# Kernel optimization log

Measured on AMD Instinct MI355X. Metric: run time of the kernel, lower is better.

## Reference

```python
import jax, jax.numpy as jnp
import numpy as np

H_DIM = 512
FF_DIM = 2048
N_HEAD = 4
N_BLOCK = 3
N_TOKEN = 128
B, S = 8, 1024
LN_EPS = 1e-5


def _layernorm(x, g, b):
    mu = jnp.mean(x, axis=-1, keepdims=True)
    var = jnp.mean(jnp.square(x - mu), axis=-1, keepdims=True)
    return (x - mu) * jax.lax.rsqrt(var + LN_EPS) * g + b


def setup_inputs() -> dict:
    key = jax.random.key(0)
    ks = jax.random.split(key, 20)
    sc = 0.02
    inp = {
        'input_ids': jax.random.randint(ks[0], (B, S), 0, N_TOKEN, dtype=jnp.int32),
        'attention_mask': jnp.ones((B, S), dtype=jnp.int32),
        'emb': jax.random.uniform(ks[1], (N_TOKEN, H_DIM), dtype=jnp.float32),
        'wq': jax.random.normal(ks[2], (N_BLOCK, N_HEAD, H_DIM, H_DIM), dtype=jnp.float32) * sc,
        'wk': jax.random.normal(ks[3], (N_BLOCK, N_HEAD, H_DIM, H_DIM), dtype=jnp.float32) * sc,
        'wv': jax.random.normal(ks[4], (N_BLOCK, N_HEAD, H_DIM, H_DIM), dtype=jnp.float32) * sc,
        'wo_w': jax.random.normal(ks[5], (N_BLOCK, N_HEAD * H_DIM, H_DIM), dtype=jnp.float32) * sc,
        'wo_b': jnp.zeros((N_BLOCK, H_DIM), dtype=jnp.float32),
        'ln1_g': jnp.ones((N_BLOCK, H_DIM), dtype=jnp.float32),
        'ln1_b': jnp.zeros((N_BLOCK, H_DIM), dtype=jnp.float32),
        'ff1_w': jax.random.normal(ks[6], (N_BLOCK, FF_DIM, H_DIM), dtype=jnp.float32) * sc,
        'ff1_b': jnp.zeros((N_BLOCK, FF_DIM), dtype=jnp.float32),
        'ff2_w': jax.random.normal(ks[7], (N_BLOCK, H_DIM, FF_DIM), dtype=jnp.float32) * sc,
        'ff2_b': jnp.zeros((N_BLOCK, H_DIM), dtype=jnp.float32),
        'ln2_g': jnp.ones((N_BLOCK, H_DIM), dtype=jnp.float32),
        'ln2_b': jnp.zeros((N_BLOCK, H_DIM), dtype=jnp.float32),
        'lm_w': jax.random.normal(ks[8], (H_DIM, N_TOKEN), dtype=jnp.float32) * sc,
    }
    return inp


def reference(emb, wq, wk, wv, wo_w, wo_b, ln1_g, ln1_b, ff1_w, ff1_b,
              ff2_w, ff2_b, ln2_g, ln2_b, lm_w, input_ids, attention_mask):
    mask_f = attention_mask.astype(jnp.float32)          # [B,S]
    valid = attention_mask != 0                          # [B,S]

    # Embedding lookup
    x = emb[input_ids]                                   # [B,S,H]

    # Positional encoding: positions assigned sequentially to valid tokens;
    # both even and odd feature slots get the SAME sin value (per source).
    pos = jnp.cumsum(mask_f, axis=-1) - 1.0              # [B,S]
    div = jnp.exp(jnp.arange(0, H_DIM, 2, dtype=jnp.float32) * (-jnp.log(10000.0) / H_DIM))  # [H/2]
    s = jnp.sin(pos[..., None] * div)                    # [B,S,H/2]
    pos_enc = jnp.repeat(s, 2, axis=-1) * mask_f[..., None]
    x = x + pos_enc

    # Allowed attention: causal (key <= query) AND query valid AND key valid
    rows = jnp.arange(S)
    causal = rows[None, :, None] >= rows[None, None, :]  # [1,S,S] (query>=key)
    allowed = causal & valid[:, :, None] & valid[:, None, :]  # [B,S,S]
    neg_inf = jnp.float32(-jnp.inf)
    scale = jnp.sqrt(jnp.float32(H_DIM))

    for l in range(N_BLOCK):
        # Per-head full-width attention (each head uses full H_DIM)
        q = jnp.einsum('bsh,nhd->bnsd', x, wq[l])
        k = jnp.einsum('bsh,nhd->bnsd', x, wk[l])
        v = jnp.einsum('bsh,nhd->bnsd', x, wv[l])
        scores = jnp.einsum('bnsd,bntd->bnst', q, k) / scale      # [B,N,S,S]
        scores = jnp.where(allowed[:, None], scores, neg_inf)
        att = jax.nn.softmax(scores, axis=-1)
        att = jnp.where(jnp.isnan(att), 0.0, att)                  # NaN rows -> 0
        o = jnp.einsum('bnst,bntd->bnsd', att, v)                  # [B,N,S,H]
        o = jnp.transpose(o, (0, 2, 1, 3)).reshape(B, S, N_HEAD * H_DIM)
        mh = o @ wo_w[l] + wo_b[l]
        x = _layernorm(x + mh, ln1_g[l], ln1_b[l])
        # Conv1d with kernel 1 == pointwise linear
        ff = jax.nn.relu(jnp.einsum('bsh,fh->bsf', x, ff1_w[l]) + ff1_b[l])
        ff = jnp.einsum('bsf,hf->bsh', ff, ff2_w[l]) + ff2_b[l]
        x = _layernorm(x + ff, ln2_g[l], ln2_b[l])

    return x @ lm_w                                       # [B,S,N_TOKEN]
```

## Files before the change

### kernel.cpp

```cpp
#include <hip/hip_runtime.h>
#include <hip/hip_bf16.h>

#define S_LEN 1024
#define BATCH 8
#define HD 512
#define FFD 2048
#define NHEAD 4
#define NBLK 3
#define NTOK 128

typedef __bf16 bf16_t;
typedef __bf16 bf16x4_t __attribute__((ext_vector_type(4)));
typedef __bf16 bf16x8_t __attribute__((ext_vector_type(8)));
typedef float f32x4_t __attribute__((ext_vector_type(4)));

typedef __attribute__((address_space(3))) uint32_t lds_u32;
typedef __attribute__((address_space(1))) uint32_t glb_u32;

template<int NI>
__device__ __forceinline__ void ldsread(const bf16_t* __restrict__ buf, int row0,
                                        int fr, int fg, int sw, bf16x8_t (&dst)[NI][2]) {
  #pragma unroll
  for (int i = 0; i < NI; ++i)
    #pragma unroll
    for (int ks = 0; ks < 2; ++ks)
      dst[i][ks] = *(const bf16x8_t*)&buf[(row0 + i*16 + fr)*64 + (((ks*4 + fg) ^ sw) << 3)];
}

template<int IB, int JB>
__device__ __forceinline__ void mquad(f32x4_t (&acc)[8][4],
                                      const bf16x8_t (&af)[4][2], const bf16x8_t (&bf)[2][2]) {
  #pragma unroll
  for (int ks = 0; ks < 2; ++ks)
    #pragma unroll
    for (int i = 0; i < 4; ++i)
      #pragma unroll
      for (int j = 0; j < 2; ++j)
        acc[IB+i][JB+j] = __builtin_amdgcn_mfma_f32_16x16x32_bf16(af[i][ks], bf[j][ks], acc[IB+i][JB+j], 0, 0, 0);
}

template<bool OUT_BF16, bool BIAS, bool RELU, bool TRI, bool CKLIM, bool NORM>
__global__ __launch_bounds__(512, 2)
void gemm256_kernel(const bf16_t* __restrict__ A,
                    const bf16_t* __restrict__ Bt,
                    const float* __restrict__ bias,
                    void* __restrict__ Cv,
                    int M, int N, int K,
                    int lda, int ldb, int ldc,
                    long long sA, long long sB, int bshift, long long sBias,
                    int zshift, long long sC_hi, long long sC_lo,
                    int msub_shift, long long msub_stride,
                    float alpha)
{
  const int zb = blockIdx.z;
  int m0, n0;
  if (TRI) {
    const int idx = blockIdx.x;
    int mi = (int)((sqrtf(8.f * idx + 1.f) - 1.f) * 0.5f);
    while ((mi + 1) * (mi + 2) / 2 <= idx) ++mi;
    while (mi * (mi + 1) / 2 > idx) --mi;
    m0 = mi * 256;
    n0 = (idx - mi * (mi + 1) / 2) * 256;
  } else {
    m0 = blockIdx.x * 256;
    n0 = blockIdx.y * 256;
  }
  int kend = K;
  if (CKLIM) { int ke = m0 + 256; kend = ke < K ? ke : K; }
  const int nt = kend >> 6;

  const bf16_t* Az = A + (long long)zb * sA;
  const bf16_t* Bz = Bt + (long long)(zb >> bshift) * sB;
  const long long coff = ((long long)(zb >> zshift)) * sC_hi
                       + ((long long)(zb & ((1 << zshift) - 1))) * sC_lo;

  __shared__ __align__(16) bf16_t As[2][256 * 64];
  __shared__ __align__(16) bf16_t Bs[2][256 * 64];

  const int tid = threadIdx.x;
  const int lane = tid & 63;
  const int w = tid >> 6;
  const int wm = (w >> 2) * 128;
  const int wn = (w & 3) * 64;
  const int fr = lane & 15;
  const int fg = lane >> 4;
  const int sw = fr & 7;

  const int srow = tid >> 3;
  const int scol8 = tid & 7;
  const int gswz = ((scol8 ^ (srow & 7)) << 3);

  f32x4_t acc[8][4];
  #pragma unroll
  for (int i = 0; i < 8; ++i)
    #pragma unroll
    for (int j = 0; j < 4; ++j)
      acc[i][j] = (f32x4_t){0.f, 0.f, 0.f, 0.f};

  const bf16_t* gA0 = Az + (long long)(m0 + srow) * lda + gswz;
  const bf16_t* gB0 = Bz + (long long)(n0 + srow) * ldb + gswz;

  auto stage_half = [&](int buf, int kt, int h) {
    if (h < 2) {
      const bf16_t* g = gA0 + (long long)(h * 128) * lda + (kt << 6);
      bf16_t* l = &As[buf][(h*128 + srow) * 64 + (scol8 << 3)];
      __builtin_amdgcn_global_load_lds((const glb_u32*)g, (lds_u32*)l, 16, 0, 0);
      __builtin_amdgcn_global_load_lds((const glb_u32*)(g + 64LL*lda), (lds_u32*)(l + 64*64), 16, 0, 0);
    } else {
      const int hh = h - 2;
      const bf16_t* g = gB0 + (long long)(hh * 128) * ldb + (kt << 6);
      bf16_t* l = &Bs[buf][(hh*128 + srow) * 64 + (scol8 << 3)];
      __builtin_amdgcn_global_load_lds((const glb_u32*)g, (lds_u32*)l, 16, 0, 0);
      __builtin_amdgcn_global_load_lds((const glb_u32*)(g + 64LL*ldb), (lds_u32*)(l + 64*64), 16, 0, 0);
    }
  };

  stage_half(0, 0, 0); stage_half(0, 0, 1); stage_half(0, 0, 2); stage_half(0, 0, 3);
  if (nt > 1) { stage_half(1, 1, 0); stage_half(1, 1, 1); }
  if (nt > 1) asm volatile("s_waitcnt vmcnt(4)" ::: "memory");
  else        asm volatile("s_waitcnt vmcnt(0)" ::: "memory");
  __builtin_amdgcn_s_barrier();
  __builtin_amdgcn_sched_barrier(0);

  for (int t = 0; t < nt; ++t) {
    const int cur = t & 1;
    const bf16_t* Ac = &As[cur][0];
    const bf16_t* Bc = &Bs[cur][0];
    bf16x8_t a0[4][2], a1[4][2], b0[2][2], b1[2][2];

    ldsread<4>(Ac, wm, fr, fg, sw, a0);
    ldsread<2>(Bc, wn, fr, fg, sw, b0);
    if (t + 1 < nt) stage_half(cur ^ 1, t + 1, 2);
    mquad<0, 0>(acc, a0, b0);
    ldsread<4>(Ac, wm + 64, fr, fg, sw, a1);
    ldsread<2>(Bc, wn + 32, fr, fg, sw, b1);
    if (t + 1 < nt) stage_half(cur ^ 1, t + 1, 3);
    mquad<4, 2>(acc, a1, b1);

    __builtin_amdgcn_s_barrier();
    __builtin_amdgcn_sched_barrier(0);

    if (t + 2 < nt) stage_half(cur, t + 2, 0);
    mquad<0, 2>(acc, a0, b1);
    if (t + 2 < nt) {
      stage_half(cur, t + 2, 1);
      asm volatile("s_waitcnt vmcnt(4)" ::: "memory");
    } else {
      asm volatile("s_waitcnt vmcnt(0)" ::: "memory");
    }
    mquad<4, 0>(acc, a1, b0);

    __builtin_amdgcn_s_barrier();
    __builtin_amdgcn_sched_barrier(0);
  }

  #pragma unroll
  for (int i = 0; i < 8; ++i) {
    #pragma unroll
    for (int e = 0; e < 4; ++e) {
      const int row = m0 + wm + i*16 + fg*4 + e;
      const long long ro = coff
        + ((long long)(row >> msub_shift)) * msub_stride
        + (long long)(row & ((1 << msub_shift) - 1)) * (long long)ldc;
      float rn = 1.f;
      if (NORM) rn = bias[(long long)zb * sBias + row];
      #pragma unroll
      for (int j = 0; j < 4; ++j) {
        const int col = n0 + wn + j*16 + fr;
        float v = acc[i][j][e] * alpha;
        if (BIAS) v += bias[(long long)zb * sBias + col];
        if (NORM) v *= rn;
        if (RELU) v = v > 0.f ? v : 0.f;
        if (OUT_BF16) ((bf16_t*)Cv)[ro + col] = (bf16_t)v;
        else          ((float*)Cv)[ro + col]  = v;
      }
    }
  }
}

template<bool OUT_BF16, bool BIAS, bool RELU, bool CSKIP, bool CKLIM>
__global__ __launch_bounds__(256, 2)
void gemm_bt_kernel(const bf16_t* __restrict__ A,
                    const bf16_t* __restrict__ Bt,
                    const float* __restrict__ bias,
                    void* __restrict__ Cv,
                    int M, int N, int K,
                    int lda, int ldb, int ldc,
                    long long sA, long long sB, int bshift, long long sBias,
                    int zshift, long long sC_hi, long long sC_lo,
                    int msub_shift, long long msub_stride,
                    float alpha)
{
  const int zb = blockIdx.z;
  const int m0 = blockIdx.x * 128;
  const int n0 = blockIdx.y * 128;
  if (CSKIP && n0 > m0 + 127) return;
  int kend = K;
  if (CKLIM) { int ke = m0 + 128; kend = ke < K ? ke : K; }

  const bf16_t* Az = A + (long long)zb * sA;
  const bf16_t* Bz = Bt + (long long)(zb >> bshift) * sB;
  const long long coff = ((long long)(zb >> zshift)) * sC_hi
                       + ((long long)(zb & ((1 << zshift) - 1))) * sC_lo;

  __shared__ __align__(16) bf16_t As[128 * 64];
  __shared__ __align__(16) bf16_t Bs[128 * 64];

  const int tid = threadIdx.x;
  const int wv = tid >> 6;
  const int lane = tid & 63;
  const int wm = (wv >> 1) * 64;
  const int wn = (wv & 1) * 64;
  const int fr = lane & 15;
  const int fg = lane >> 4;
  const int sw = fr & 7;

  f32x4_t acc[4][4];
  #pragma unroll
  for (int i = 0; i < 4; ++i)
    #pragma unroll
    for (int j = 0; j < 4; ++j)
      acc[i][j] = (f32x4_t){0.f, 0.f, 0.f, 0.f};

  const bf16_t* ga = Az + (long long)(m0 + (wv << 5) + (lane >> 3)) * lda
                   + (((lane & 7) ^ (lane >> 3)) << 3);
  const bf16_t* gb = Bz + (long long)(n0 + (wv << 5) + (lane >> 3)) * ldb
                   + (((lane & 7) ^ (lane >> 3)) << 3);

  for (int k0 = 0; k0 < kend; k0 += 64) {
    #pragma unroll
    for (int s = 0; s < 4; ++s) {
      __builtin_amdgcn_global_load_lds(
        (const glb_u32*)(ga + (long long)s * 8 * lda + k0),
        (lds_u32*)(As + (wv * 4 + s) * 512), 16, 0, 0);
      __builtin_amdgcn_global_load_lds(
        (const glb_u32*)(gb + (long long)s * 8 * ldb + k0),
        (lds_u32*)(Bs + (wv * 4 + s) * 512), 16, 0, 0);
    }
    __syncthreads();
    #pragma unroll
    for (int kc = 0; kc < 2; ++kc) {
      const int ca = ((kc * 4 + fg) ^ sw) << 3;
      bf16x8_t af[4], bfr[4];
      #pragma unroll
      for (int i = 0; i < 4; ++i)
        af[i] = *(const bf16x8_t*)&As[(wm + i*16 + fr) * 64 + ca];
      #pragma unroll
      for (int j = 0; j < 4; ++j)
        bfr[j] = *(const bf16x8_t*)&Bs[(wn + j*16 + fr) * 64 + ca];
      #pragma unroll
      for (int i = 0; i < 4; ++i)
        #pragma unroll
        for (int j = 0; j < 4; ++j)
          acc[i][j] = __builtin_amdgcn_mfma_f32_16x16x32_bf16(af[i], bfr[j], acc[i][j], 0, 0, 0);
    }
    __syncthreads();
  }

  #pragma unroll
  for (int i = 0; i < 4; ++i) {
    #pragma unroll
    for (int e = 0; e < 4; ++e) {
      const int row = m0 + wm + i*16 + fg*4 + e;
      const long long ro = coff
        + ((long long)(row >> msub_shift)) * msub_stride
        + (long long)(row & ((1 << msub_shift) - 1)) * (long long)ldc;
      #pragma unroll
      for (int j = 0; j < 4; ++j) {
        const int col = n0 + wn + j*16 + fr;
        float v = acc[i][j][e] * alpha;
        if (BIAS) v += bias[(long long)zb * sBias + col];
        if (RELU) v = v > 0.f ? v : 0.f;
        if (OUT_BF16) ((bf16_t*)Cv)[ro + col] = (bf16_t)v;
        else          ((float*)Cv)[ro + col]  = v;
      }
    }
  }
}

__global__ void softmax_kernel(bf16_t* __restrict__ scP,
                               const int* __restrict__ mask, int pair0)
{
  const int lane = threadIdx.x & 63;
  const int s = blockIdx.x * 4 + (threadIdx.x >> 6);
  const int pz = blockIdx.y;
  const int b = (pair0 + pz) >> 2;
  bf16_t* row = scP + ((long long)pz * S_LEN + s) * S_LEN;
  const int t0 = lane * 16;

  bf16x8_t r0 = *(const bf16x8_t*)&row[t0];
  bf16x8_t r1 = *(const bf16x8_t*)&row[t0 + 8];
  int4 m4[4];
  #pragma unroll
  for (int q = 0; q < 4; ++q) m4[q] = *(const int4*)&mask[b * S_LEN + t0 + q*4];
  const int* mm = (const int*)m4;

  float v[16]; bool ok[16];
  #pragma unroll
  for (int j = 0; j < 16; ++j) {
    const int t = t0 + j;
    ok[j] = (t <= s) && (mm[j] != 0);
    float raw = (j < 8) ? (float)r0[j] : (float)r1[j - 8];
    v[j] = ok[j] ? raw : -INFINITY;
  }
  float mx = v[0];
  #pragma unroll
  for (int j = 1; j < 16; ++j) mx = fmaxf(mx, v[j]);
  #pragma unroll
  for (int o = 32; o; o >>= 1) mx = fmaxf(mx, __shfl_xor(mx, o));

  float e[16]; float sum = 0.f;
  #pragma unroll
  for (int j = 0; j < 16; ++j) { e[j] = ok[j] ? __expf(v[j] - mx) : 0.f; sum += e[j]; }
  #pragma unroll
  for (int o = 32; o; o >>= 1) sum += __shfl_xor(sum, o);

  const bool qvalid = mask[b * S_LEN + s] != 0;
  const float inv = (qvalid && sum > 0.f) ? 1.f / sum : 0.f;
  bf16x8_t o0, o1;
  #pragma unroll
  for (int j = 0; j < 8; ++j) { o0[j] = (bf16_t)(e[j] * inv); o1[j] = (bf16_t)(e[j+8] * inv); }
  *(bf16x8_t*)&row[t0] = o0;
  *(bf16x8_t*)&row[t0 + 8] = o1;
}

template<typename TIN>
__global__ void transpose_kernel(const TIN* __restrict__ in, bf16_t* __restrict__ out,
                                 int R, int C, long long sIn, long long sOut)
{
  __shared__ float tile[32][33];
  const long long zi = (long long)blockIdx.z * sIn;
  const long long zo = (long long)blockIdx.z * sOut;
  const int c0 = blockIdx.x * 32, r0 = blockIdx.y * 32;
  const int tx = threadIdx.x, ty = threadIdx.y;
  #pragma unroll
  for (int i = 0; i < 4; ++i) {
    int r = r0 + ty + i*8;
    tile[ty + i*8][tx] = (float)in[zi + (long long)r * C + c0 + tx];
  }
  __syncthreads();
  #pragma unroll
  for (int i = 0; i < 4; ++i) {
    int c = c0 + ty + i*8;
    out[zo + (long long)c * R + r0 + tx] = (bf16_t)tile[tx][ty + i*8];
  }
}

__global__ void convert2_kernel(const float* __restrict__ a, const float* __restrict__ b,
                                bf16_t* __restrict__ out, long long n)
{
  long long i = (long long)blockIdx.x * blockDim.x + threadIdx.x;
  long long stride = (long long)gridDim.x * blockDim.x;
  for (; i < 2*n; i += stride)
    out[i] = (bf16_t)(i < n ? a[i] : b[i - n]);
}

__global__ void fill_kernel(float* __restrict__ out, long long n, float v)
{
  long long i = (long long)blockIdx.x * blockDim.x + threadIdx.x;
  long long stride = (long long)gridDim.x * blockDim.x;
  for (; i < n; i += stride) out[i] = v;
}

__global__ void pos_kernel(const int* __restrict__ mask, float* __restrict__ pos)
{
  __shared__ float scn[S_LEN];
  const int b = blockIdx.x, t = threadIdx.x;
  scn[t] = (float)(mask[b * S_LEN + t] != 0);
  __syncthreads();
  for (int off = 1; off < S_LEN; off <<= 1) {
    float add = (t >= off) ? scn[t - off] : 0.f;
    __syncthreads();
    scn[t] += add;
    __syncthreads();
  }
  pos[b * S_LEN + t] = scn[t] - 1.0f;
}

__global__ void embed_kernel(const int* __restrict__ ids, const int* __restrict__ mask,
                             const float* __restrict__ pos, const float* __restrict__ emb,
                             float* __restrict__ x, bf16_t* __restrict__ xb)
{
  const int idx = blockIdx.x * 256 + threadIdx.x;
  const int i = idx & 255;
  const int bs = idx >> 8;
  const int id = ids[bs];
  const float m = (float)(mask[bs] != 0);
  const float p = pos[bs];
  const float dv = __expf(-(float)(2 * i) * (9.210340371976184f / (float)HD));
  const float sv = __sinf(p * dv) * m;
  const float e0 = emb[id * HD + 2*i], e1 = emb[id * HD + 2*i + 1];
  const float x0 = e0 + sv, x1 = e1 + sv;
  x[(long long)bs * HD + 2*i]     = x0;
  x[(long long)bs * HD + 2*i + 1] = x1;
  xb[(long long)bs * HD + 2*i]     = (bf16_t)x0;
  xb[(long long)bs * HD + 2*i + 1] = (bf16_t)x1;
}

__global__ void ln_kernel(float* __restrict__ x, const float* __restrict__ tparts,
                          int ns, long long pstride,
                          const float* __restrict__ bias,
                          const float* __restrict__ g, const float* __restrict__ b,
                          bf16_t* __restrict__ xb)
{
  const int lane = threadIdx.x & 63;
  const long long row = (long long)blockIdx.x * 4 + (threadIdx.x >> 6);
  const int e0 = lane * 8;
  const long long base = row * HD + e0;

  float4 xa = *(const float4*)&x[base];
  float4 xc = *(const float4*)&x[base + 4];
  float4 ba = *(const float4*)&bias[e0];
  float4 bc = *(const float4*)&bias[e0 + 4];
  float v[8] = {xa.x+ba.x, xa.y+ba.y, xa.z+ba.z, xa.w+ba.w,
                xc.x+bc.x, xc.y+bc.y, xc.z+bc.z, xc.w+bc.w};
  for (int i = 0; i < ns; ++i) {
    float4 p0 = *(const float4*)&tparts[i*pstride + base];
    float4 p1 = *(const float4*)&tparts[i*pstride + base + 4];
    v[0]+=p0.x; v[1]+=p0.y; v[2]+=p0.z; v[3]+=p0.w;
    v[4]+=p1.x; v[5]+=p1.y; v[6]+=p1.z; v[7]+=p1.w;
  }
  float s = 0.f;
  #pragma unroll
  for (int j = 0; j < 8; ++j) s += v[j];
  #pragma unroll
  for (int o = 32; o; o >>= 1) s += __shfl_xor(s, o);
  const float mu = s * (1.f / (float)HD);
  float q = 0.f;
  #pragma unroll
  for (int j = 0; j < 8; ++j) { v[j] -= mu; q += v[j]*v[j]; }
  #pragma unroll
  for (int o = 32; o; o >>= 1) q += __shfl_xor(q, o);
  const float inv = rsqrtf(q * (1.f / (float)HD) + 1e-5f);

  float4 ga4 = *(const float4*)&g[e0];
  float4 gc4 = *(const float4*)&g[e0 + 4];
  float4 bb4 = *(const float4*)&b[e0];
  float4 bd4 = *(const float4*)&b[e0 + 4];
  float y[8] = {v[0]*inv*ga4.x+bb4.x, v[1]*inv*ga4.y+bb4.y, v[2]*inv*ga4.z+bb4.z, v[3]*inv*ga4.w+bb4.w,
                v[4]*inv*gc4.x+bd4.x, v[5]*inv*gc4.y+bd4.y, v[6]*inv*gc4.z+bd4.z, v[7]*inv*gc4.w+bd4.w};
  *(float4*)&x[base]     = (float4){y[0],y[1],y[2],y[3]};
  *(float4*)&x[base + 4] = (float4){y[4],y[5],y[6],y[7]};
  bf16x8_t yb;
  #pragma unroll
  for (int j = 0; j < 8; ++j) yb[j] = (bf16_t)y[j];
  *(bf16x8_t*)&xb[base] = yb;
}

__global__ void lnb_kernel(float* __restrict__ x, const bf16_t* __restrict__ tparts,
                           long long pstride,
                           const float* __restrict__ bias,
                           const float* __restrict__ g, const float* __restrict__ b,
                           bf16_t* __restrict__ xb)
{
  const int lane = threadIdx.x & 63;
  const long long row = (long long)blockIdx.x * 4 + (threadIdx.x >> 6);
  const int e0 = lane * 8;
  const long long base = row * HD + e0;

  float4 xa = *(const float4*)&x[base];
  float4 xc = *(const float4*)&x[base + 4];
  float4 ba = *(const float4*)&bias[e0];
  float4 bc = *(const float4*)&bias[e0 + 4];
  float v[8] = {xa.x+ba.x, xa.y+ba.y, xa.z+ba.z, xa.w+ba.w,
                xc.x+bc.x, xc.y+bc.y, xc.z+bc.z, xc.w+bc.w};
  #pragma unroll
  for (int i = 0; i < 4; ++i) {
    bf16x8_t pp = *(const bf16x8_t*)&tparts[i*pstride + base];
    #pragma unroll
    for (int j = 0; j < 8; ++j) v[j] += (float)pp[j];
  }
  float s = 0.f;
  #pragma unroll
  for (int j = 0; j < 8; ++j) s += v[j];
  #pragma unroll
  for (int o = 32; o; o >>= 1) s += __shfl_xor(s, o);
  const float mu = s * (1.f / (float)HD);
  float q = 0.f;
  #pragma unroll
  for (int j = 0; j < 8; ++j) { v[j] -= mu; q += v[j]*v[j]; }
  #pragma unroll
  for (int o = 32; o; o >>= 1) q += __shfl_xor(q, o);
  const float inv = rsqrtf(q * (1.f / (float)HD) + 1e-5f);

  float4 ga4 = *(const float4*)&g[e0];
  float4 gc4 = *(const float4*)&g[e0 + 4];
  float4 bb4 = *(const float4*)&b[e0];
  float4 bd4 = *(const float4*)&b[e0 + 4];
  float y[8] = {v[0]*inv*ga4.x+bb4.x, v[1]*inv*ga4.y+bb4.y, v[2]*inv*ga4.z+bb4.z, v[3]*inv*ga4.w+bb4.w,
                v[4]*inv*gc4.x+bd4.x, v[5]*inv*gc4.y+bd4.y, v[6]*inv*gc4.z+bd4.z, v[7]*inv*gc4.w+bd4.w};
  *(float4*)&x[base]     = (float4){y[0],y[1],y[2],y[3]};
  *(float4*)&x[base + 4] = (float4){y[4],y[5],y[6],y[7]};
  bf16x8_t yb;
  #pragma unroll
  for (int j = 0; j < 8; ++j) yb[j] = (bf16_t)y[j];
  *(bf16x8_t*)&xb[base] = yb;
}

extern "C" void kernel_launch(void* const* d_in, const int* in_sizes, int n_in,
                              void* d_out, int out_size, void* d_ws, size_t ws_size,
                              hipStream_t stream)
{
  (void)in_sizes; (void)n_in;
  const int*   ids   = (const int*)d_in[0];
  const int*   amask = (const int*)d_in[1];
  const float* emb   = (const float*)d_in[2];
  const float* wq    = (const float*)d_in[3];
  const float* wk    = (const float*)d_in[4];
  const float* wv    = (const float*)d_in[5];
  const float* wo_w  = (const float*)d_in[6];
  const float* wo_b  = (const float*)d_in[7];
  const float* ln1_g = (const float*)d_in[8];
  const float* ln1_b = (const float*)d_in[9];
  const float* ff1_w = (const float*)d_in[10];
  const float* ff1_b = (const float*)d_in[11];
  const float* ff2_w = (const float*)d_in[12];
  const float* ff2_b = (const float*)d_in[13];
  const float* ln2_g = (const float*)d_in[14];
  const float* ln2_b = (const float*)d_in[15];
  const float* lm_w  = (const float*)d_in[16];

  const long long MROW = (long long)BATCH * S_LEN;
  const size_t MBc = 1ull << 20;
  char* p = (char*)d_ws;
  auto alloc = [&](size_t bytes) { char* r = p; p += (bytes + 255) & ~(size_t)255; return r; };

  float*  x     = (float*) alloc(MROW * HD * 4);
  bf16_t* xb    = (bf16_t*)alloc(MROW * HD * 2);
  bf16_t* ob    = (bf16_t*)alloc(4LL * MROW * HD * 2);
  bf16_t* wqkb  = (bf16_t*)alloc(8LL * HD * HD * 2);
  bf16_t* wvb   = (bf16_t*)alloc(4LL * HD * HD * 2);
  bf16_t* Gt    = (bf16_t*)alloc(4LL * HD * HD * 2);
  bf16_t* UT    = (bf16_t*)alloc(4LL * HD * HD * 2);
  bf16_t* woT   = (bf16_t*)alloc((long long)HD * FFD * 2);
  bf16_t* wff1  = (bf16_t*)alloc((long long)FFD * HD * 2);
  bf16_t* wff2  = (bf16_t*)alloc((long long)HD * FFD * 2);
  bf16_t* lmT   = (bf16_t*)alloc((long long)NTOK * HD * 2);
  float*  pos   = (float*) alloc(MROW * 4);

  const size_t used = (size_t)(p - (char*)d_ws);
  const size_t rem  = ws_size > used ? ws_size - used : 0;

  int P = 0, SK = 2;
  if      (rem >= 128 * MBc) { P = 32; SK = 4; }
  else if (rem >= 64 * MBc)  { P = 8;  SK = 2; }
  if (P == 0) {
    fill_kernel<<<1024, 256, 0, stream>>>((float*)d_out, (long long)out_size,
                                          (float)(ws_size >> 20));
    return;
  }

  char* A = p;
  const long long pairE = (long long)S_LEN * HD;
  bf16_t* qc  = (bf16_t*)A;
  bf16_t* uTc = qc  + (long long)P * pairE;
  bf16_t* scb = uTc + (long long)P * pairE;
  float*  tmp = (float*)A;
  bf16_t* ffb = (bf16_t*)(A + (size_t)SK * 16 * MBc);

  const dim3 tb(32, 8);
  transpose_kernel<float><<<dim3(4,16,1), tb, 0, stream>>>(lm_w, lmT, HD, NTOK, 0, 0);
  pos_kernel<<<BATCH, S_LEN, 0, stream>>>(amask, pos);
  embed_kernel<<<8192, 256, 0, stream>>>(ids, amask, pos, emb, x, xb);

  const int nch = 32 / P;
  const int bpc = P / NHEAD;

  for (int l = 0; l < NBLK; ++l) {
    convert2_kernel<<<2048, 256, 0, stream>>>(
      wq + (long long)l*NHEAD*HD*HD, wk + (long long)l*NHEAD*HD*HD, wqkb, 4LL*HD*HD);
    convert2_kernel<<<2048, 256, 0, stream>>>(
      wv + (long long)l*NHEAD*HD*HD, wv + (long long)l*NHEAD*HD*HD + 2LL*HD*HD,
      wvb, 2LL*HD*HD);
    transpose_kernel<float><<<dim3(16,64,1), tb, 0, stream>>>(
      wo_w + (long long)l*FFD*HD, woT, FFD, HD, 0, 0);
    convert2_kernel<<<2048, 256, 0, stream>>>(
      ff1_w + (long long)l*FFD*HD, ff2_w + (long long)l*HD*FFD, wff1, (long long)FFD*HD);
    gemm_bt_kernel<true,false,false,false,false><<<dim3(4,4,4),256,0,stream>>>(
      wqkb + 4LL*HD*HD, wqkb, nullptr, Gt,
      HD, HD, HD, HD, HD, HD,
      (long long)HD*HD, (long long)HD*HD, 0, 0,
      30, 0, (long long)HD*HD,
      30, 0, 1.f);
    gemm_bt_kernel<true,false,false,false,false><<<dim3(4,4,4),256,0,stream>>>(
      woT, wvb, nullptr, UT,
      HD, HD, HD, FFD, HD, HD,
      512, (long long)HD*HD, 0, 0,
      30, 0, (long long)HD*HD,
      30, 0, 1.f);

    for (int c = 0; c < nch; ++c) {
      const int b0 = c * bpc;
      const int pair0 = b0 * NHEAD;
      const int Mch = bpc * S_LEN;

      gemm256_kernel<true,false,false,false,false,false><<<dim3(Mch/256,2,4),512,0,stream>>>(
        xb + (long long)b0*S_LEN*HD, Gt, nullptr, qc, Mch, HD, HD, HD, HD, HD,
        0, (long long)HD*HD, 0, 0,
        2, 0, pairE,
        10, (long long)NHEAD*pairE, 1.f);

      gemm256_kernel<true,false,false,false,false,false><<<dim3(8,4,bpc),512,0,stream>>>(
        UT, xb + (long long)b0*S_LEN*HD, nullptr, uTc,
        2048, S_LEN, HD, HD, HD, S_LEN,
        0, (long long)S_LEN*HD, 0, 0,
        0, (long long)NHEAD*HD*S_LEN, 0,
        9, (long long)HD*S_LEN, 1.f);

      gemm_bt_kernel<true,false,false,true,false><<<dim3(8,8,P),256,0,stream>>>(
        qc, xb + (long long)b0*S_LEN*HD, nullptr, scb,
        S_LEN, S_LEN, HD, HD, HD, S_LEN,
        pairE, (long long)S_LEN*HD, 2, 0,
        30, 0, (long long)S_LEN*S_LEN,
        30, 0, 0.044194173824159216f);
      softmax_kernel<<<dim3(S_LEN/4,P),256,0,stream>>>(scb, amask, pair0);
      gemm256_kernel<true,false,false,false,true,false><<<dim3(4,2,P),512,0,stream>>>(
        scb, uTc, nullptr, ob,
        S_LEN, HD, S_LEN, S_LEN, S_LEN, HD,
        (long long)S_LEN*S_LEN, (long long)HD*S_LEN, 0, 0,
        2, (long long)S_LEN*HD, (long long)MROW*HD,
        30, 0, 1.f);
    }

    lnb_kernel<<<2048,256,0,stream>>>(x, ob, (long long)MROW*HD,
                                      wo_b + l*HD, ln1_g + l*HD, ln1_b + l*HD, xb);

    gemm256_kernel<true,true,true,false,false,false><<<dim3(32,8,1),512,0,stream>>>(
      xb, wff1, ff1_b + l*FFD, ffb,
      (int)MROW, FFD, HD, HD, HD, FFD,
      0, 0, 0, 0, 30, 0, 0, 30, 0, 1.f);
    gemm256_kernel<false,false,false,false,false,false><<<dim3(32,2,SK),512,0,stream>>>(
      ffb, wff2, nullptr, tmp,
      (int)MROW, HD, FFD/SK, FFD, FFD, HD,
      FFD/SK, FFD/SK, 0, 0,
      0, (long long)MROW*HD, 0,
      30, 0, 1.f);
    ln_kernel<<<2048,256,0,stream>>>(x, tmp, SK, (long long)MROW*HD,
                                     ff2_b + l*HD, ln2_g + l*HD, ln2_b + l*HD, xb);
  }

  gemm_bt_kernel<false,false,false,false,false><<<dim3(64,1,1),256,0,stream>>>(
    xb, lmT, nullptr, (float*)d_out,
    (int)MROW, NTOK, HD, HD, HD, NTOK,
    0, 0, 0, 0, 30, 0, 0, 30, 0, 1.f);
}
```

Before: 796.1 us.

## Split causal attention-times-V GEMM along K to balance work across blocks

Adds a KSPLIT mode to the 256-tile GEMM that splits the causal-limited K range of the P·V product into two halves, each written to separate partial output slices. Lower row tiles skip the upper half and return early. The layernorm kernel then sums eight partials for rows in the second half of the sequence instead of four. The aim is to even out the imbalance from causal K-limiting, where late row tiles do up to four times the work of early ones. The cost is more launched blocks, a doubled partial buffer, and extra reads in the layernorm for those rows.

```diff
diff --git a/kernel.cpp b/kernel.cpp
--- a/kernel.cpp
+++ b/kernel.cpp
@@ -39,7 +39,7 @@
         acc[IB+i][JB+j] = __builtin_amdgcn_mfma_f32_16x16x32_bf16(af[i][ks], bf[j][ks], acc[IB+i][JB+j], 0, 0, 0);
 }
 
-template<bool OUT_BF16, bool BIAS, bool RELU, bool TRI, bool CKLIM, bool NORM>
+template<bool OUT_BF16, bool BIAS, bool RELU, bool TRI, bool CKLIM, bool NORM, bool KSPLIT>
 __global__ __launch_bounds__(512, 2)
 void gemm256_kernel(const bf16_t* __restrict__ A,
                     const bf16_t* __restrict__ Bt,
@@ -53,6 +53,8 @@
                     float alpha)
 {
   const int zb = blockIdx.z;
+  int pair = zb, khh = 0;
+  if (KSPLIT) { pair = zb & ((1 << bshift) - 1); khh = zb >> bshift; }
   int m0, n0;
   if (TRI) {
     const int idx = blockIdx.x;
@@ -66,13 +68,20 @@
     n0 = blockIdx.y * 256;
   }
   int kend = K;
-  if (CKLIM) { int ke = m0 + 256; kend = ke < K ? ke : K; }
+  if (CKLIM) {
+    int ke = m0 + 256;
+    int kcap = (KSPLIT && khh == 0) ? (K >> 1) : K;
+    kend = ke < kcap ? ke : kcap;
+  }
+  const int t0 = (KSPLIT && khh) ? (K >> 7) : 0;
+  if (KSPLIT && kend <= (t0 << 6)) return;
   const int nt = kend >> 6;
 
-  const bf16_t* Az = A + (long long)zb * sA;
-  const bf16_t* Bz = Bt + (long long)(zb >> bshift) * sB;
-  const long long coff = ((long long)(zb >> zshift)) * sC_hi
-                       + ((long long)(zb & ((1 << zshift) - 1))) * sC_lo;
+  const bf16_t* Az = A + (long long)(KSPLIT ? pair : zb) * sA;
+  const bf16_t* Bz = Bt + (long long)(KSPLIT ? pair : (zb >> bshift)) * sB;
+  long long coff = ((long long)(pair >> zshift)) * sC_hi
+                 + ((long long)(pair & ((1 << zshift) - 1))) * sC_lo;
+  if (KSPLIT) coff += (long long)khh * sBias;
 
   __shared__ __align__(16) bf16_t As[2][256 * 64];
   __shared__ __align__(16) bf16_t Bs[2][256 * 64];
@@ -115,15 +124,15 @@
     }
   };
 
-  stage_half(0, 0, 0); stage_half(0, 0, 1); stage_half(0, 0, 2); stage_half(0, 0, 3);
-  if (nt > 1) { stage_half(1, 1, 0); stage_half(1, 1, 1); }
-  if (nt > 1) asm volatile("s_waitcnt vmcnt(4)" ::: "memory");
-  else        asm volatile("s_waitcnt vmcnt(0)" ::: "memory");
+  stage_half(0, t0, 0); stage_half(0, t0, 1); stage_half(0, t0, 2); stage_half(0, t0, 3);
+  if (nt - t0 > 1) { stage_half(1, t0 + 1, 0); stage_half(1, t0 + 1, 1); }
+  if (nt - t0 > 1) asm volatile("s_waitcnt vmcnt(4)" ::: "memory");
+  else             asm volatile("s_waitcnt vmcnt(0)" ::: "memory");
   __builtin_amdgcn_s_barrier();
   __builtin_amdgcn_sched_barrier(0);
 
-  for (int t = 0; t < nt; ++t) {
-    const int cur = t & 1;
+  for (int t = t0; t < nt; ++t) {
+    const int cur = (t - t0) & 1;
     const bf16_t* Ac = &As[cur][0];
     const bf16_t* Bc = &Bs[cur][0];
     bf16x8_t a0[4][2], a1[4][2], b0[2][2], b1[2][2];
@@ -163,12 +172,12 @@
         + ((long long)(row >> msub_shift)) * msub_stride
         + (long long)(row & ((1 << msub_shift) - 1)) * (long long)ldc;
       float rn = 1.f;
-      if (NORM) rn = bias[(long long)zb * sBias + row];
+      if (NORM) rn = bias[(long long)pair * sBias + row];
       #pragma unroll
       for (int j = 0; j < 4; ++j) {
         const int col = n0 + wn + j*16 + fr;
         float v = acc[i][j][e] * alpha;
-        if (BIAS) v += bias[(long long)zb * sBias + col];
+        if (BIAS) v += bias[(long long)pair * sBias + col];
         if (NORM) v *= rn;
         if (RELU) v = v > 0.f ? v : 0.f;
         if (OUT_BF16) ((bf16_t*)Cv)[ro + col] = (bf16_t)v;
@@ -448,7 +457,7 @@
 }
 
 __global__ void lnb_kernel(float* __restrict__ x, const bf16_t* __restrict__ tparts,
-                           long long pstride,
+                           long long pstride, int nsl_hi,
                            const float* __restrict__ bias,
                            const float* __restrict__ g, const float* __restrict__ b,
                            bf16_t* __restrict__ xb)
@@ -457,6 +466,8 @@
   const long long row = (long long)blockIdx.x * 4 + (threadIdx.x >> 6);
   const int e0 = lane * 8;
   const long long base = row * HD + e0;
+  const int s_in_seq = (int)(row & (S_LEN - 1));
+  const int nsl = (s_in_seq >= 512) ? nsl_hi : 4;
 
   float4 xa = *(const float4*)&x[base];
   float4 xc = *(const float4*)&x[base + 4];
@@ -464,8 +475,7 @@
   float4 bc = *(const float4*)&bias[e0 + 4];
   float v[8] = {xa.x+ba.x, xa.y+ba.y, xa.z+ba.z, xa.w+ba.w,
                 xc.x+bc.x, xc.y+bc.y, xc.z+bc.z, xc.w+bc.w};
-  #pragma unroll
-  for (int i = 0; i < 4; ++i) {
+  for (int i = 0; i < nsl; ++i) {
     bf16x8_t pp = *(const bf16x8_t*)&tparts[i*pstride + base];
     #pragma unroll
     for (int j = 0; j < 8; ++j) v[j] += (float)pp[j];
@@ -527,7 +537,7 @@
 
   float*  x     = (float*) alloc(MROW * HD * 4);
   bf16_t* xb    = (bf16_t*)alloc(MROW * HD * 2);
-  bf16_t* ob    = (bf16_t*)alloc(4LL * MROW * HD * 2);
+  bf16_t* ob    = (bf16_t*)alloc(8LL * MROW * HD * 2);
   bf16_t* wqkb  = (bf16_t*)alloc(8LL * HD * HD * 2);
   bf16_t* wvb   = (bf16_t*)alloc(4LL * HD * HD * 2);
   bf16_t* Gt    = (bf16_t*)alloc(4LL * HD * HD * 2);
@@ -594,13 +604,13 @@
       const int pair0 = b0 * NHEAD;
       const int Mch = bpc * S_LEN;
 
-      gemm256_kernel<true,false,false,false,false,false><<<dim3(Mch/256,2,4),512,0,stream>>>(
+      gemm256_kernel<true,false,false,false,false,false,false><<<dim3(Mch/256,2,4),512,0,stream>>>(
         xb + (long long)b0*S_LEN*HD, Gt, nullptr, qc, Mch, HD, HD, HD, HD, HD,
         0, (long long)HD*HD, 0, 0,
         2, 0, pairE,
         10, (long long)NHEAD*pairE, 1.f);
 
-      gemm256_kernel<true,false,false,false,false,false><<<dim3(8,4,bpc),512,0,stream>>>(
+      gemm256_kernel<true,false,false,false,false,false,false><<<dim3(8,4,bpc),512,0,stream>>>(
         UT, xb + (long long)b0*S_LEN*HD, nullptr, uTc,
         2048, S_LEN, HD, HD, HD, S_LEN,
         0, (long long)S_LEN*HD, 0, 0,
@@ -614,22 +624,32 @@
         30, 0, (long long)S_LEN*S_LEN,
         30, 0, 0.044194173824159216f);
       softmax_kernel<<<dim3(S_LEN/4,P),256,0,stream>>>(scb, amask, pair0);
-      gemm256_kernel<true,false,false,false,true,false><<<dim3(4,2,P),512,0,stream>>>(
-        scb, uTc, nullptr, ob,
-        S_LEN, HD, S_LEN, S_LEN, S_LEN, HD,
-        (long long)S_LEN*S_LEN, (long long)HD*S_LEN, 0, 0,
-        2, (long long)S_LEN*HD, (long long)MROW*HD,
-        30, 0, 1.f);
+
+      if (P == 32) {
+        gemm256_kernel<true,false,false,false,true,false,true><<<dim3(4,2,64),512,0,stream>>>(
+          scb, uTc, nullptr, ob,
+          S_LEN, HD, S_LEN, S_LEN, S_LEN, HD,
+          (long long)S_LEN*S_LEN, (long long)HD*S_LEN, 5, 4LL*MROW*HD,
+          2, (long long)S_LEN*HD, (long long)MROW*HD,
+          30, 0, 1.f);
+      } else {
+        gemm256_kernel<true,false,false,false,true,false,false><<<dim3(4,2,P),512,0,stream>>>(
+          scb, uTc, nullptr, ob + (long long)b0*S_LEN*HD,
+          S_LEN, HD, S_LEN, S_LEN, S_LEN, HD,
+          (long long)S_LEN*S_LEN, (long long)HD*S_LEN, 0, 0,
+          2, (long long)S_LEN*HD, (long long)MROW*HD,
+          30, 0, 1.f);
+      }
     }
 
-    lnb_kernel<<<2048,256,0,stream>>>(x, ob, (long long)MROW*HD,
+    lnb_kernel<<<2048,256,0,stream>>>(x, ob, (long long)MROW*HD, (P == 32) ? 8 : 4,
                                       wo_b + l*HD, ln1_g + l*HD, ln1_b + l*HD, xb);
 
-    gemm256_kernel<true,true,true,false,false,false><<<dim3(32,8,1),512,0,stream>>>(
+    gemm256_kernel<true,true,true,false,false,false,false><<<dim3(32,8,1),512,0,stream>>>(
       xb, wff1, ff1_b + l*FFD, ffb,
       (int)MROW, FFD, HD, HD, HD, FFD,
       0, 0, 0, 0, 30, 0, 0, 30, 0, 1.f);
-    gemm256_kernel<false,false,false,false,false,false><<<dim3(32,2,SK),512,0,stream>>>(
+    gemm256_kernel<false,false,false,false,false,false,false><<<dim3(32,2,SK),512,0,stream>>>(
       ffb, wff2, nullptr, tmp,
       (int)MROW, HD, FFD/SK, FFD, FFD, HD,
       FFD/SK, FFD/SK, 0, 0,
```

Result: slower. 845.9 us (+6.3%).
